# Kernel optimization log

Hardware: AMD Instinct MI355X
Metric: run time of the kernel (lower is better)

Reference implementation:

```python
import jax, jax.numpy as jnp
import numpy as np

IMG = 416                      # image_shape
DIST = 1075.0                  # isocenter_distance
N_ANG = 320                    # 360 / rotation_resolution(=1.125 deg)
N_DET = IMG                    # detector bins
N_SAMP = IMG                   # integration samples per ray
SCALE = 512.0 / 416.0 * 0.03   # self.scale


def _ray_coords():
    """Pixel-space sample coordinates for every (angle, detector, sample).
    Returns cols, rows of shape [N_ANG, N_DET, N_SAMP] and the step length dt."""
    thetas = (jnp.arange(N_ANG, dtype=jnp.float32) * np.float32(2.0 * np.pi / N_ANG))
    half_diag = (IMG / 2.0) * np.sqrt(2.0)
    gamma_max = np.float32(np.arcsin(half_diag / DIST))  # half fan angle covering image
    gammas = jnp.linspace(-gamma_max, gamma_max, N_DET, dtype=jnp.float32)
    ray_len = np.float32(IMG * np.sqrt(2.0))             # chord length through image
    ts = jnp.linspace(np.float32(DIST - ray_len / 2.0),
                      np.float32(DIST + ray_len / 2.0), N_SAMP, dtype=jnp.float32)
    dt = float(ray_len / (N_SAMP - 1))

    th = thetas[:, None, None]        # [A,1,1]
    gm = gammas[None, :, None]        # [1,D,1]
    t = ts[None, None, :]             # [1,1,S]
    # source position on circle of radius DIST, ray direction toward detector
    sx = np.float32(DIST) * jnp.cos(th)
    sy = np.float32(DIST) * jnp.sin(th)
    x = sx - t * jnp.cos(th + gm)     # [A,D,S] world coords (isocenter at origin)
    y = sy - t * jnp.sin(th + gm)
    ctr = np.float32((IMG - 1) / 2.0)
    return x + ctr, y + ctr, dt       # pixel (col, row) coordinates


def _bilinear(img, cols, rows):
    """Zero-padded bilinear sampling of img[H,W] at float (row,col) coords."""
    c0 = jnp.floor(cols)
    r0 = jnp.floor(rows)
    wc = cols - c0
    wr = rows - r0
    c0i = c0.astype(jnp.int32)
    r0i = r0.astype(jnp.int32)

    def g(ri, ci):
        inb = (ri >= 0) & (ri < IMG) & (ci >= 0) & (ci < IMG)
        v = img[jnp.clip(ri, 0, IMG - 1), jnp.clip(ci, 0, IMG - 1)]
        return jnp.where(inb, v, jnp.float32(0.0))

    return (g(r0i, c0i) * (1 - wr) * (1 - wc)
            + g(r0i, c0i + 1) * (1 - wr) * wc
            + g(r0i + 1, c0i) * wr * (1 - wc)
            + g(r0i + 1, c0i + 1) * wr * wc)


def fan_beam_fp(vol):
    """vol: [B,H,W] -> sinogram [B, N_ANG, N_DET] via ray integration."""
    cols, rows, dt = _ray_coords()
    proj_one = lambda img: _bilinear(img, cols, rows).sum(axis=-1) * jnp.float32(dt)
    return jax.vmap(proj_one)(vol)


def setup_inputs() -> dict:
    key = jax.random.key(0)
    k1, k2 = jax.random.split(key)
    inp = jax.random.normal(k1, (1, 1, IMG, IMG), dtype=jnp.float32)
    tgt = jax.random.normal(k2, (1, 1, IMG, IMG), dtype=jnp.float32)
    return {"input": inp, "target": tgt}


def reference(input, target):
    input_proj = fan_beam_fp(input[:, 0])   # squeeze(1)
    target_proj = fan_beam_fp(target[:, 0])
    return jnp.mean((input_proj - target_proj) ** 2) * jnp.float32(SCALE)
```

## Files before the change

### kernel.cpp

```cpp
#include <hip/hip_runtime.h>
#include <math.h>

#define IMG 416
#define N_ANG 320
#define N_DET 416
#define N_SAMP 416
#define NK (N_SAMP / 8)

#define TW 105
#define TABLE_WORDS (TW * TW * 16)
#define TBYTES ((size_t)TABLE_WORDS * 4)

typedef float vfloat2 __attribute__((ext_vector_type(2)));

__global__ __launch_bounds__(256) void pack_kernel(const float* __restrict__ a,
                                                   const float* __restrict__ b,
                                                   unsigned int* __restrict__ T,
                                                   float* __restrict__ out) {
    int i = blockIdx.x * 256 + threadIdx.x;
    if (i == 0) out[0] = 0.0f;
    if (i >= TABLE_WORDS) return;
    int tile = i >> 4, sub = i & 15;
    int tr = tile / TW, tc = tile - tr * TW;
    int pr = tr * 4 + (sub >> 2);
    int pc = tc * 4 + (sub & 3);
    int r = pr - 1, c = pc - 1;
    float v00 = 0.f, v01 = 0.f, v10 = 0.f, v11 = 0.f;
    bool c0in = (unsigned)c < (unsigned)IMG;
    bool c1in = (unsigned)(c + 1) < (unsigned)IMG;
    if ((unsigned)r < (unsigned)IMG) {
        int base = r * IMG;
        if (c0in) v00 = a[base + c] - b[base + c];
        if (c1in) v01 = a[base + c + 1] - b[base + c + 1];
    }
    if ((unsigned)(r + 1) < (unsigned)IMG) {
        int base = (r + 1) * IMG;
        if (c0in) v10 = a[base + c] - b[base + c];
        if (c1in) v11 = a[base + c + 1] - b[base + c + 1];
    }
    unsigned int u = __builtin_amdgcn_cvt_pk_fp8_f32(v00, v01, 0u, false);
    u = __builtin_amdgcn_cvt_pk_fp8_f32(v10, v11, u, true);
    T[i] = u;
}

__global__ void zero_out_kernel(float* __restrict__ out) {
    if (threadIdx.x == 0) out[0] = 0.0f;
}

__global__ __launch_bounds__(256) void proj_packed(const unsigned int* __restrict__ T,
                                                   float* __restrict__ out,
                                                   float theta_step, float gmax,
                                                   float gstep, float t0,
                                                   float dtstep, float coef) {
    const int lane = threadIdx.x & 63;
    const int wave = (blockIdx.x * 256 + threadIdx.x) >> 6;
    const int det_base = wave << 3;
    const int a  = det_base / N_DET;
    const int d  = det_base - a * N_DET + (lane >> 3);
    const int s0 = lane & 7;

    const float theta = (float)a * theta_step;
    const float gamma = fmaf((float)d, gstep, -gmax);
    float s1, c1, s2, c2;
    sincosf(theta, &s1, &c1);
    sincosf(theta + gamma, &s2, &c2);
    const float sx = fmaf(1075.0f, c1, 207.5f);
    const float sy = fmaf(1075.0f, s1, 207.5f);

    const float dt8 = 8.0f * dtstep;
    const float tstart = fmaf((float)s0, dtstep, t0);

    const float c2g = (fabsf(c2) < 1e-12f) ? 1e-12f : c2;
    const float s2g = (fabsf(s2) < 1e-12f) ? 1e-12f : s2;
    const float ix = 1.0f / c2g, iy = 1.0f / s2g;
    const float tax = (sx - 416.5f) * ix, tbx = (sx + 1.5f) * ix;
    const float tay = (sy - 416.5f) * iy, tby = (sy + 1.5f) * iy;
    const float t_lo = fmaxf(fminf(tax, tbx), fminf(tay, tby));
    const float t_hi = fminf(fmaxf(tax, tbx), fmaxf(tay, tby));

    const float inv_dt8 = 1.0f / dt8;
    int klo = (int)floorf((t_lo - tstart) * inv_dt8);
    int khi = (int)ceilf((t_hi - tstart) * inv_dt8);
    klo = max(0, min(klo, NK));
    khi = min(NK - 1, khi);

    #pragma unroll
    for (int m = 1; m < 64; m <<= 1) {
        klo = min(klo, __shfl_xor(klo, m, 64));
        khi = max(khi, __shfl_xor(khi, m, 64));
    }
    klo = __builtin_amdgcn_readfirstlane(klo);
    khi = __builtin_amdgcn_readfirstlane(khi);

    const float tb = fmaf((float)klo, dt8, tstart);
    float colp = fmaf(-tb, c2, sx + 1.0f);
    float rowp = fmaf(-tb, s2, sy + 1.0f);
    const float dcol = -dt8 * c2;
    const float drow = -dt8 * s2;

    float acc = 0.0f;
    #pragma unroll 4
    for (int k = klo; k <= khi; ++k) {
        const float colc = fminf(fmaxf(colp, 0.0f), 417.5f);
        const float rowc = fminf(fmaxf(rowp, 0.0f), 417.5f);
        const int pc = (int)colc;
        const int pr = (int)rowc;
        const float wc = colc - (float)pc;
        const float wr = rowc - (float)pr;

        const int idx = (((pr >> 2) * TW + (pc >> 2)) << 4) + ((pr & 3) << 2) + (pc & 3);
        const unsigned int u = T[idx];
        const vfloat2 lo = __builtin_amdgcn_cvt_pk_f32_fp8(u, false);
        const vfloat2 hi = __builtin_amdgcn_cvt_pk_f32_fp8(u, true);

        const float top = fmaf(wc, lo[1] - lo[0], lo[0]);
        const float bot = fmaf(wc, hi[1] - hi[0], hi[0]);
        acc = fmaf(wr, bot - top, acc + top);

        colp += dcol;
        rowp += drow;
    }

    #pragma unroll
    for (int m = 1; m < 8; m <<= 1) acc += __shfl_xor(acc, m, 64);
    float sq = acc * acc;
    #pragma unroll
    for (int m = 8; m < 64; m <<= 1) sq += __shfl_xor(sq, m, 64);

    __shared__ float wsum[4];
    if (lane == 0) wsum[threadIdx.x >> 6] = sq;
    __syncthreads();
    if (threadIdx.x == 0)
        atomicAdd(out, (wsum[0] + wsum[1] + wsum[2] + wsum[3]) * coef);
}

__global__ __launch_bounds__(256) void proj_fused(const float* __restrict__ imgA,
                                                  const float* __restrict__ imgB,
                                                  float* __restrict__ out,
                                                  float theta_step, float gmax,
                                                  float gstep, float t0,
                                                  float dtstep, float coef) {
    const int idx = blockIdx.x * 256 + threadIdx.x;
    const int a  = idx / N_DET;
    const int dd = idx - a * N_DET;
    const float theta = (float)a * theta_step;
    const float gamma = fmaf((float)dd, gstep, -gmax);
    float s1, c1, s2, c2;
    sincosf(theta, &s1, &c1);
    sincosf(theta + gamma, &s2, &c2);
    const float sx = 1075.0f * c1 + 207.5f;
    const float sy = 1075.0f * s1 + 207.5f;
    float acc = 0.0f;
    #pragma unroll 4
    for (int s = 0; s < N_SAMP; ++s) {
        const float t   = fmaf((float)s, dtstep, t0);
        const float col = fmaf(-t, c2, sx);
        const float row = fmaf(-t, s2, sy);
        const float c0 = floorf(col);
        const float r0 = floorf(row);
        const float wc = col - c0;
        const float wr = row - r0;
        const int ci = (int)c0;
        const int ri = (int)r0;
        auto G = [&](int r, int c) -> float {
            if ((unsigned)r < (unsigned)IMG && (unsigned)c < (unsigned)IMG)
                return imgA[r * IMG + c] - imgB[r * IMG + c];
            return 0.0f;
        };
        const float v00 = G(ri, ci);
        const float v01 = G(ri, ci + 1);
        const float v10 = G(ri + 1, ci);
        const float v11 = G(ri + 1, ci + 1);
        const float top = fmaf(wc, v01 - v00, v00);
        const float bot = fmaf(wc, v11 - v10, v10);
        acc += fmaf(wr, bot - top, top);
    }
    float sq = acc * acc;
    #pragma unroll
    for (int o = 32; o > 0; o >>= 1) sq += __shfl_down(sq, o, 64);
    __shared__ float wsum[4];
    const int lane = threadIdx.x & 63;
    if (lane == 0) wsum[threadIdx.x >> 6] = sq;
    __syncthreads();
    if (threadIdx.x == 0)
        atomicAdd(out, (wsum[0] + wsum[1] + wsum[2] + wsum[3]) * coef);
}

extern "C" void kernel_launch(void* const* d_in, const int* in_sizes, int n_in,
                              void* d_out, int out_size, void* d_ws, size_t ws_size,
                              hipStream_t stream) {
    const float* in = (const float*)d_in[0];
    const float* tg = (const float*)d_in[1];
    float* out = (float*)d_out;

    const double half_diag = (IMG / 2.0) * sqrt(2.0);
    const double ray_len   = IMG * sqrt(2.0);
    const float  gmax      = (float)asin(half_diag / 1075.0);
    const float  gstep     = (float)(2.0 * (double)gmax / (N_DET - 1));
    const float  t0        = (float)(1075.0 - ray_len / 2.0);
    const float  dtstep    = (float)(ray_len / (N_SAMP - 1));
    const float  theta_step = (float)(2.0 * M_PI / N_ANG);
    const double dt        = ray_len / (N_SAMP - 1);
    const double SCALE     = 512.0 / 416.0 * 0.03;
    const float  coef      = (float)(dt * dt * SCALE / ((double)N_ANG * N_DET));

    const int n_rays = N_ANG * N_DET;
    if (ws_size >= TBYTES) {
        unsigned int* T = (unsigned int*)d_ws;
        pack_kernel<<<(TABLE_WORDS + 255) / 256, 256, 0, stream>>>(in, tg, T, out);
        proj_packed<<<(n_rays / 8) / 4, 256, 0, stream>>>(
            T, out, theta_step, gmax, gstep, t0, dtstep, coef);
    } else {
        zero_out_kernel<<<1, 64, 0, stream>>>(out);
        proj_fused<<<n_rays / 256, 256, 0, stream>>>(
            in, tg, out, theta_step, gmax, gstep, t0, dtstep, coef);
    }
}
```

Before: 113.8 us.

## Use padded linear FP8 table with 16.16 fixed-point ray stepping

Replaces the 4x4-tiled FP8 difference table with a row-major table padded by 33 pixels on each side and a power-of-two row stride of 512. The inner loop now steps ray positions in 16.16 fixed point, so the byte address comes from shifts and masks and the clamping and float-to-int conversions go away. The sample range is tightened to the padded bounds and the unroll factor goes from 4 to 8. The trade-offs are a larger table to build, the loss of tile locality for the 2D gathers, and fixed-point rounding drift over long rays.

```diff
diff --git a/kernel.cpp b/kernel.cpp
--- a/kernel.cpp
+++ b/kernel.cpp
@@ -7,9 +7,11 @@
 #define N_SAMP 416
 #define NK (N_SAMP / 8)
 
-#define TW 105
-#define TABLE_WORDS (TW * TW * 16)
+#define TROWS 484
+#define TSTRIDE 512
+#define TABLE_WORDS (TROWS * TSTRIDE)
 #define TBYTES ((size_t)TABLE_WORDS * 4)
+#define PADOFF 33.0f
 
 typedef float vfloat2 __attribute__((ext_vector_type(2)));
 
@@ -20,11 +22,9 @@
     int i = blockIdx.x * 256 + threadIdx.x;
     if (i == 0) out[0] = 0.0f;
     if (i >= TABLE_WORDS) return;
-    int tile = i >> 4, sub = i & 15;
-    int tr = tile / TW, tc = tile - tr * TW;
-    int pr = tr * 4 + (sub >> 2);
-    int pc = tc * 4 + (sub & 3);
-    int r = pr - 1, c = pc - 1;
+    int pr = i >> 9;
+    int pc = i & 511;
+    int r = pr - 33, c = pc - 33;
     float v00 = 0.f, v01 = 0.f, v10 = 0.f, v11 = 0.f;
     bool c0in = (unsigned)c < (unsigned)IMG;
     bool c1in = (unsigned)(c + 1) < (unsigned)IMG;
@@ -64,8 +64,8 @@
     float s1, c1, s2, c2;
     sincosf(theta, &s1, &c1);
     sincosf(theta + gamma, &s2, &c2);
-    const float sx = fmaf(1075.0f, c1, 207.5f);
-    const float sy = fmaf(1075.0f, s1, 207.5f);
+    const float sx = fmaf(1075.0f, c1, 207.5f + PADOFF);
+    const float sy = fmaf(1075.0f, s1, 207.5f + PADOFF);
 
     const float dt8 = 8.0f * dtstep;
     const float tstart = fmaf((float)s0, dtstep, t0);
@@ -73,14 +73,14 @@
     const float c2g = (fabsf(c2) < 1e-12f) ? 1e-12f : c2;
     const float s2g = (fabsf(s2) < 1e-12f) ? 1e-12f : s2;
     const float ix = 1.0f / c2g, iy = 1.0f / s2g;
-    const float tax = (sx - 416.5f) * ix, tbx = (sx + 1.5f) * ix;
-    const float tay = (sy - 416.5f) * iy, tby = (sy + 1.5f) * iy;
+    const float tax = (sx - 450.5f) * ix, tbx = (sx - 31.5f) * ix;
+    const float tay = (sy - 450.5f) * iy, tby = (sy - 31.5f) * iy;
     const float t_lo = fmaxf(fminf(tax, tbx), fminf(tay, tby));
     const float t_hi = fminf(fmaxf(tax, tbx), fmaxf(tay, tby));
 
     const float inv_dt8 = 1.0f / dt8;
-    int klo = (int)floorf((t_lo - tstart) * inv_dt8);
-    int khi = (int)ceilf((t_hi - tstart) * inv_dt8);
+    int klo = (int)ceilf((t_lo - tstart) * inv_dt8 - 1e-3f);
+    int khi = (int)floorf((t_hi - tstart) * inv_dt8 + 1e-3f);
     klo = max(0, min(klo, NK));
     khi = min(NK - 1, khi);
 
@@ -93,23 +93,23 @@
     khi = __builtin_amdgcn_readfirstlane(khi);
 
     const float tb = fmaf((float)klo, dt8, tstart);
-    float colp = fmaf(-tb, c2, sx + 1.0f);
-    float rowp = fmaf(-tb, s2, sy + 1.0f);
-    const float dcol = -dt8 * c2;
-    const float drow = -dt8 * s2;
-
+    const float colp0 = fmaf(-tb, c2, sx);
+    const float rowp0 = fmaf(-tb, s2, sy);
+    int colf = (int)(colp0 * 65536.0f);
+    int rowf = (int)(rowp0 * 65536.0f);
+    const int dc = (int)floorf(-dt8 * c2 * 65536.0f + 0.5f);
+    const int dr = (int)floorf(-dt8 * s2 * 65536.0f + 0.5f);
+
+    const char* __restrict__ Tb = (const char*)T;
     float acc = 0.0f;
-    #pragma unroll 4
+    #pragma unroll 8
     for (int k = klo; k <= khi; ++k) {
-        const float colc = fminf(fmaxf(colp, 0.0f), 417.5f);
-        const float rowc = fminf(fmaxf(rowp, 0.0f), 417.5f);
-        const int pc = (int)colc;
-        const int pr = (int)rowc;
-        const float wc = colc - (float)pc;
-        const float wr = rowc - (float)pr;
-
-        const int idx = (((pr >> 2) * TW + (pc >> 2)) << 4) + ((pr & 3) << 2) + (pc & 3);
-        const unsigned int u = T[idx];
+        const int addr = ((rowf >> 5) & 0x000FF800) | ((colf >> 14) & 0x7FC);
+        const unsigned int u = *(const unsigned int*)(Tb + addr);
+
+        const float wc = (float)(colf & 0xffff) * 0x1p-16f;
+        const float wr = (float)(rowf & 0xffff) * 0x1p-16f;
+
         const vfloat2 lo = __builtin_amdgcn_cvt_pk_f32_fp8(u, false);
         const vfloat2 hi = __builtin_amdgcn_cvt_pk_f32_fp8(u, true);
 
@@ -117,8 +117,8 @@
         const float bot = fmaf(wc, hi[1] - hi[0], hi[0]);
         acc = fmaf(wr, bot - top, acc + top);
 
-        colp += dcol;
-        rowp += drow;
+        colf += dc;
+        rowf += dr;
     }
 
     #pragma unroll
@@ -207,7 +207,7 @@
     const int n_rays = N_ANG * N_DET;
     if (ws_size >= TBYTES) {
         unsigned int* T = (unsigned int*)d_ws;
-        pack_kernel<<<(TABLE_WORDS + 255) / 256, 256, 0, stream>>>(in, tg, T, out);
+        pack_kernel<<<TABLE_WORDS / 256, 256, 0, stream>>>(in, tg, T, out);
         proj_packed<<<(n_rays / 8) / 4, 256, 0, stream>>>(
             T, out, theta_step, gmax, gstep, t0, dtstep, coef);
     } else {
```

Result: no change. 115.4 us (+1.4%).
